# Performance work log

Measured on AMD Instinct MI355X. Metric: run time of the kernel, lower is better.

The kernel has to match this reference:

```python
import jax, jax.numpy as jnp
import numpy as np
from jax import lax

EPS = 1e-5
NPOINT, NSAMPLE = 1024, 32

def bn(x, g, b, m, v):
    # inference-mode batchnorm over last (channel) axis
    return (x - m) * (g * lax.rsqrt(v + EPS)) + b

def gather_pts(points, idx):
    # points [B,N,C], idx [B,...] -> [B,...,C]
    return jax.vmap(lambda p, i: p[i])(points, idx)

def fps(xyz, npoint):
    # iterative farthest point sampling, deterministic start at index 0
    B, N, _ = xyz.shape
    xyz = lax.stop_gradient(xyz)
    def step(carry, _):
        dist, far = carry
        centroid = jnp.take_along_axis(xyz, far[:, None, None], axis=1)  # [B,1,3]
        d = jnp.sum((xyz - centroid) ** 2, -1)                           # [B,N]
        dist = jnp.minimum(dist, d)
        return (dist, jnp.argmax(dist, -1)), far
    init = (jnp.full((B, N), 1e10, xyz.dtype), jnp.zeros((B,), jnp.int32))
    _, idxs = lax.scan(step, init, None, length=npoint)
    return idxs.T  # [B,npoint]

def setup_inputs():
    key = jax.random.key(0)
    ks = jax.random.split(key, 8)
    d = {"x": jax.random.normal(ks[0], (8, 8192, 3), jnp.float32)}
    d["conv1_w"] = jax.random.normal(ks[1], (64, 3), jnp.float32) * 0.3
    d["conv2_w"] = jax.random.normal(ks[2], (64, 64), jnp.float32) * 0.1
    d["lconv1_w"] = jax.random.normal(ks[3], (128, 128), jnp.float32) * 0.08
    d["lconv2_w"] = jax.random.normal(ks[4], (128, 128), jnp.float32) * 0.08
    for name, c, k in (("bn1", 64, ks[5]), ("bn2", 64, ks[6]), ("lbn1", 128, ks[7]), ("lbn2", 128, jax.random.fold_in(key, 99))):
        d[name + "_g"] = jax.random.uniform(k, (c,), jnp.float32, 0.5, 1.5)
        d[name + "_b"] = jax.random.normal(jax.random.fold_in(k, 1), (c,), jnp.float32) * 0.1
        d[name + "_m"] = jnp.zeros((c,), jnp.float32)
        d[name + "_v"] = jnp.ones((c,), jnp.float32)
    return d

def reference(x, conv1_w, conv2_w, lconv1_w, lconv2_w,
              bn1_g, bn1_b, bn1_m, bn1_v, bn2_g, bn2_b, bn2_m, bn2_v,
              lbn1_g, lbn1_b, lbn1_m, lbn1_v, lbn2_g, lbn2_b, lbn2_m, lbn2_v):
    xyz = x[..., :3]                                                    # [B,N,3]
    f = jax.nn.relu(bn(jnp.einsum("bnd,ed->bne", x, conv1_w), bn1_g, bn1_b, bn1_m, bn1_v))
    f = jax.nn.relu(bn(jnp.einsum("bne,fe->bnf", f, conv2_w), bn2_g, bn2_b, bn2_m, bn2_v))  # [B,N,64]
    # sample_and_group(npoint=1024, nsample=32)
    fps_idx = fps(xyz, NPOINT)                                          # [B,S]
    new_xyz = gather_pts(xyz, fps_idx)                                  # [B,S,3]
    new_pts = gather_pts(f, fps_idx)                                    # [B,S,64]
    d2 = (jnp.sum(new_xyz ** 2, -1)[:, :, None] + jnp.sum(xyz ** 2, -1)[:, None, :]
          - 2.0 * jnp.einsum("bsd,bnd->bsn", new_xyz, xyz))             # [B,S,N]
    knn_idx = lax.top_k(-d2, NSAMPLE)[1]                                # [B,S,K] smallest dists
    grouped = gather_pts(f, knn_idx)                                    # [B,S,K,64]
    centered = grouped - new_pts[:, :, None, :]
    feat = jnp.concatenate([centered, jnp.broadcast_to(new_pts[:, :, None, :], grouped.shape)], -1)  # [B,S,K,128]
    # Local_op: two 1x1 conv + BN + relu, max over K
    h = jax.nn.relu(bn(jnp.einsum("bskd,ed->bske", feat, lconv1_w), lbn1_g, lbn1_b, lbn1_m, lbn1_v))
    h = jax.nn.relu(bn(jnp.einsum("bske,fe->bskf", h, lconv2_w), lbn2_g, lbn2_b, lbn2_m, lbn2_v))
    feature_0 = jnp.transpose(jnp.max(h, axis=2), (0, 2, 1))            # [B,128,S]
    return (new_xyz, feature_0, new_xyz, feature_0)
```

## Files before the change

kernel.cpp:

```cpp
#include <hip/hip_runtime.h>
#include <hip/hip_bf16.h>
#include <math.h>
#include <stdint.h>

#define EPS_BN 1e-5f

constexpr int Nx = 8192;
constexpr int NP = 1024;
constexpr int NWORK = 248;
constexpr int NEMB  = 128;
#define POISON_I ((int)0xAAAAAAAA)

typedef __attribute__((ext_vector_type(8))) __bf16 bf16x8;
typedef __attribute__((ext_vector_type(4))) float  f32x4;
typedef __attribute__((ext_vector_type(2))) float  f32x2;
typedef unsigned int uint32;
typedef unsigned long long u64;

template<int CTRL, int RMASK>
__device__ __forceinline__ u64 dpp_max_u64(u64 k) {
    uint32 klo = (uint32)k, khi = (uint32)(k >> 32);
    uint32 plo = (uint32)__builtin_amdgcn_update_dpp((int)klo, (int)klo, CTRL, RMASK, 0xf, false);
    uint32 phi = (uint32)__builtin_amdgcn_update_dpp((int)khi, (int)khi, CTRL, RMASK, 0xf, false);
    u64 p = ((u64)phi << 32) | plo;
    return (p > k) ? p : k;
}
__device__ __forceinline__ u64 wave_max_u64(u64 k) {
    k = dpp_max_u64<0x111, 0xf>(k);
    k = dpp_max_u64<0x112, 0xf>(k);
    k = dpp_max_u64<0x114, 0xf>(k);
    k = dpp_max_u64<0x118, 0xf>(k);
    k = dpp_max_u64<0x142, 0xa>(k);
    k = dpp_max_u64<0x143, 0xc>(k);
    uint32 rlo = (uint32)__builtin_amdgcn_readlane((int)(uint32)k, 63);
    uint32 rhi = (uint32)__builtin_amdgcn_readlane((int)(k >> 32), 63);
    return ((u64)rhi << 32) | rlo;
}
template<int CTRL, int RMASK>
__device__ __forceinline__ int dpp_sum_i32(int c) {
    int t = __builtin_amdgcn_update_dpp(0, c, CTRL, RMASK, 0xf, true);
    return c + t;
}
__device__ __forceinline__ int wave_sum_i32(int c) {
    c = dpp_sum_i32<0x111, 0xf>(c);
    c = dpp_sum_i32<0x112, 0xf>(c);
    c = dpp_sum_i32<0x114, 0xf>(c);
    c = dpp_sum_i32<0x118, 0xf>(c);
    c = dpp_sum_i32<0x142, 0xa>(c);
    c = dpp_sum_i32<0x143, 0xc>(c);
    return __builtin_amdgcn_readlane(c, 63);
}
template<int CTRL, int RMASK>
__device__ __forceinline__ int dpp_min_i32(int v) {
    int t = __builtin_amdgcn_update_dpp(v, v, CTRL, RMASK, 0xf, false);
    return min(v, t);
}
__device__ __forceinline__ int wave_min_i32(int v) {
    v = dpp_min_i32<0x111, 0xf>(v);
    v = dpp_min_i32<0x112, 0xf>(v);
    v = dpp_min_i32<0x114, 0xf>(v);
    v = dpp_min_i32<0x118, 0xf>(v);
    v = dpp_min_i32<0x142, 0xa>(v);
    v = dpp_min_i32<0x143, 0xc>(v);
    return __builtin_amdgcn_readlane(v, 63);
}

__global__ __launch_bounds__(512, 1) void mega_kernel(
    const float* __restrict__ x,
    const float* __restrict__ w1, const float* __restrict__ w2,
    const float* g1, const float* b1, const float* m1, const float* v1,
    const float* g2, const float* b2, const float* m2, const float* v2,
    const float* __restrict__ lw1, const float* __restrict__ lw2,
    const float* lg1, const float* lb1, const float* lm1, const float* lv1,
    const float* lg2, const float* lb2, const float* lm2, const float* lv2,
    float* __restrict__ f, float4* __restrict__ pts4, int* fpsI, int* done,
    float* __restrict__ out0, float* __restrict__ out1,
    float* __restrict__ out2, float* __restrict__ out3)
{
    __shared__ __attribute__((aligned(16))) char smemRaw[131200];
    int tid = threadIdx.x;

    if (blockIdx.x < 8) {
#pragma clang fp contract(off)
        float4* xyzL = (float4*)smemRaw;
        u64*    redK = (u64*)(smemRaw + 131072);
        int b = blockIdx.x;
        int wid = tid >> 6, lane = tid & 63;
        const float* xb = x + (size_t)b * Nx * 3;
        f32x2 px[8], py[8], pz[8], dist[8];
        {
            const float4* xv = (const float4*)(xb + tid * 48);
            float F[48];
#pragma unroll
            for (int q = 0; q < 12; q++) {
                float4 v = xv[q];
                F[q*4+0]=v.x; F[q*4+1]=v.y; F[q*4+2]=v.z; F[q*4+3]=v.w;
            }
#pragma unroll
            for (int i = 0; i < 8; i++) {
                px[i] = (f32x2){F[(2*i)*3+0], F[(2*i+1)*3+0]};
                py[i] = (f32x2){F[(2*i)*3+1], F[(2*i+1)*3+1]};
                pz[i] = (f32x2){F[(2*i)*3+2], F[(2*i+1)*3+2]};
                dist[i] = (f32x2){1e10f, 1e10f};
            }
#pragma unroll
            for (int j = 0; j < 16; j++) {
                int jj = (j + (tid & 15)) & 15;
                xyzL[tid*16 + jj] = make_float4(F[jj*3], F[jj*3+1], F[jj*3+2], 0.f);
            }
        }
        __syncthreads();
        int far = 0;
        for (int st = 0; st < NP; st++) {
            float4 c = xyzL[far];
            if (tid == 0) {
                __hip_atomic_store(&fpsI[b*NP + st], far, __ATOMIC_RELAXED, __HIP_MEMORY_SCOPE_AGENT);
                int o = (b*NP + st) * 3;
                out0[o]=c.x; out0[o+1]=c.y; out0[o+2]=c.z;
                out2[o]=c.x; out2[o+1]=c.y; out2[o+2]=c.z;
            }
            f32x2 cx = {c.x, c.x}, cy = {c.y, c.y}, cz = {c.z, c.z};
            f32x2 bv2 = {-1.0f, -1.0f};
#pragma unroll
            for (int i = 0; i < 8; i++) {
                f32x2 dx = px[i] - cx, dy = py[i] - cy, dz = pz[i] - cz;
                f32x2 sq = (dx*dx + dy*dy) + dz*dz;
                f32x2 dm = __builtin_elementwise_min(dist[i], sq);
                dist[i] = dm;
                bv2 = __builtin_elementwise_max(bv2, dm);
            }
            float bv = fmaxf(bv2.x, bv2.y);
            int bi = 0;
#pragma unroll
            for (int i = 7; i >= 0; i--) {
                if (dist[i].y == bv) bi = tid*16 + 2*i + 1;
                if (dist[i].x == bv) bi = tid*16 + 2*i;
            }
            u64 bk = ((u64)__float_as_uint(bv) << 32) | (uint32)(~bi);
            bk = wave_max_u64(bk);
            if (lane == 0) redK[(st & 1)*8 + wid] = bk;
            __syncthreads();
            u64 mx = redK[(st & 1)*8 + 0];
#pragma unroll
            for (int i = 1; i < 8; i++) {
                u64 t2 = redK[(st & 1)*8 + i];
                if (t2 > mx) mx = t2;
            }
            far = (int)(~(uint32)mx);
        }
        return;
    }

    int wb = (int)blockIdx.x - 8;

    if (wb < NEMB) {
        float*  W1L = (float*)smemRaw;
        float4* W2L = (float4*)(smemRaw + 1024);
        float*  s1L = (float*)(smemRaw + 17408);
        float*  m1L = (float*)(smemRaw + 17664);
        float*  b1L = (float*)(smemRaw + 17920);
        float*  s2L = (float*)(smemRaw + 18176);
        float*  m2L = (float*)(smemRaw + 18432);
        float*  b2L = (float*)(smemRaw + 18688);
        if (tid < 192) W1L[tid] = w1[tid];
        for (int i = tid; i < 1024; i += 512) W2L[i] = ((const float4*)w2)[i];
        if (tid < 64) {
            s1L[tid] = g1[tid] * (1.0f / sqrtf(v1[tid] + EPS_BN));
            m1L[tid] = m1[tid];  b1L[tid] = b1[tid];
            s2L[tid] = g2[tid] * (1.0f / sqrtf(v2[tid] + EPS_BN));
            m2L[tid] = m2[tid];  b2L[tid] = b2[tid];
        }
        __syncthreads();
        int n = wb * 512 + tid;
        const float* xp = x + (size_t)n * 3;
        float x0 = xp[0], x1 = xp[1], x2 = xp[2];
        {
#pragma clang fp contract(off)
            float nv = (x0 * x0 + x1 * x1) + x2 * x2;
            pts4[n] = make_float4(x0, x1, x2, nv);
        }
        float t[64];
#pragma unroll
        for (int e = 0; e < 64; e++) {
            float v = fmaf(x2, W1L[e*3+2], fmaf(x1, W1L[e*3+1], x0 * W1L[e*3]));
            v = (v - m1L[e]) * s1L[e] + b1L[e];
            t[e] = fmaxf(v, 0.0f);
        }
        float acc[64];
#pragma unroll
        for (int o = 0; o < 64; o++) acc[o] = 0.0f;
#pragma unroll
        for (int e4 = 0; e4 < 16; e4++) {
            float a0 = t[e4*4], a1 = t[e4*4+1], a2 = t[e4*4+2], a3 = t[e4*4+3];
#pragma unroll
            for (int o = 0; o < 64; o++) {
                float4 w = W2L[o*16 + e4];
                acc[o] = fmaf(a3, w.w, fmaf(a2, w.z, fmaf(a1, w.y, fmaf(a0, w.x, acc[o]))));
            }
        }
        float4* fo = (float4*)(f + (size_t)n * 64);
#pragma unroll
        for (int q = 0; q < 16; q++) {
            float r0 = fmaxf((acc[q*4+0] - m2L[q*4+0]) * s2L[q*4+0] + b2L[q*4+0], 0.f);
            float r1 = fmaxf((acc[q*4+1] - m2L[q*4+1]) * s2L[q*4+1] + b2L[q*4+1], 0.f);
            float r2 = fmaxf((acc[q*4+2] - m2L[q*4+2]) * s2L[q*4+2] + b2L[q*4+2], 0.f);
            float r3 = fmaxf((acc[q*4+3] - m2L[q*4+3]) * s2L[q*4+3] + b2L[q*4+3], 0.f);
            fo[q] = make_float4(r0, r1, r2, r3);
        }
        __syncthreads();
        if (tid == 0)
            __hip_atomic_fetch_add(done, 1, __ATOMIC_RELEASE, __HIP_MEMORY_SCOPE_AGENT);
    }

    __bf16* featL = (__bf16*)smemRaw;
    __bf16* h1L   = (__bf16*)(smemRaw + 8704);
    float*  cf    = (float*) (smemRaw + 17408);
    int*    rowL  = (int*)   (smemRaw + 17664);
    int*    redC  = (int*)   (smemRaw + 17792);
    int*    redM  = (int*)   (smemRaw + 17856);
    int*    misc  = (int*)   (smemRaw + 17920);

    int wv = tid >> 6, lane = tid & 63;
    int l15 = lane & 15, quad = lane >> 4;
    int nbase = wv * 16;
    const f32x4 vzero = {0.f, 0.f, 0.f, 0.f};

    bf16x8 bf1[4], bf2[4];
#pragma unroll
    for (int kt = 0; kt < 4; kt++) {
        const float* p1 = lw1 + (size_t)(nbase + l15) * 128 + kt*32 + quad*8;
        const float* p2 = lw2 + (size_t)(nbase + l15) * 128 + kt*32 + quad*8;
        bf16x8 a1, a2;
#pragma unroll
        for (int j = 0; j < 8; j++) { a1[j] = (__bf16)p1[j]; a2[j] = (__bf16)p2[j]; }
        bf1[kt] = a1; bf2[kt] = a2;
    }
    int oc = nbase + l15;
    float sc1 = lg1[oc] * (1.0f / sqrtf(lv1[oc] + EPS_BN));
    float mm1 = lm1[oc], bb1 = lb1[oc];
    float sc2 = lg2[oc] * (1.0f / sqrtf(lv2[oc] + EPS_BN));
    float mm2 = lm2[oc], bb2 = lb2[oc];

    if (tid == 0) {
        while (__hip_atomic_load(done, __ATOMIC_RELAXED, __HIP_MEMORY_SCOPE_AGENT) != POISON_I + NEMB)
            __builtin_amdgcn_s_sleep(8);
    }
    __syncthreads();
    __threadfence();

    for (int t = wb; t < 8192; t += NWORK) {
        int b = t & 7, s = t >> 3;
        int q = (b << 10) | s;
        if (tid == 0) {
            int v;
            while ((v = __hip_atomic_load(&fpsI[q], __ATOMIC_RELAXED, __HIP_MEMORY_SCOPE_AGENT)) < 0)
                __builtin_amdgcn_s_sleep(2);
            misc[1] = v;
            misc[0] = 0;
        }
        __syncthreads();
        int cIdx = misc[1];
        if (tid < 16) {
            float4 v = *(const float4*)(f + ((size_t)b * Nx + cIdx) * 64 + tid * 4);
            cf[tid*4]=v.x; cf[tid*4+1]=v.y; cf[tid*4+2]=v.z; cf[tid*4+3]=v.w;
        }
        uint32 key[16];
        {
#pragma clang fp contract(off)
            const float4* P = pts4 + (size_t)b * Nx;
            float4 qp = P[cIdx];
#pragma unroll
            for (int i = 0; i < 16; i++) {
                int n = tid + (i << 9);
                float4 p = P[n];
                float dot = (qp.x * p.x + qp.y * p.y) + qp.z * p.z;
                float d = (qp.w + p.w) - 2.0f * dot;
                uint32 u = __float_as_uint(d);
                key[i] = (u & 0x80000000u) ? ~u : (u | 0x80000000u);
            }
        }
        uint32 prefix = 0; int krem = 32;
        for (int bit = 31; bit >= 0; bit--) {
            uint32 sv = prefix >> bit;
            int cnt = 0;
#pragma unroll
            for (int i = 0; i < 16; i++)
                cnt += ((key[i] >> bit) == sv) ? 1 : 0;
            cnt = wave_sum_i32(cnt);
            if (lane == 0) redC[(bit & 1)*8 + wv] = cnt;
            __syncthreads();
            int total = 0;
#pragma unroll
            for (int j = 0; j < 8; j++) total += redC[(bit & 1)*8 + j];
            if (total < krem) { prefix |= (1u << bit); krem -= total; }
        }
#pragma unroll
        for (int i = 0; i < 16; i++) {
            if (key[i] < prefix) {
                int pos = atomicAdd(&misc[0], 1);
                rowL[pos] = tid + (i << 9);
            }
        }
        __syncthreads();
        int last = -1;
        for (int tt = 0; tt < krem; tt++) {
            int local = 0x7fffffff;
#pragma unroll
            for (int i = 0; i < 16; i++) {
                int n = tid + (i << 9);
                if (key[i] == prefix && n > last && n < local) local = n;
            }
            local = wave_min_i32(local);
            if (lane == 0) redM[(tt & 1)*8 + wv] = local;
            __syncthreads();
            int g = 0x7fffffff;
#pragma unroll
            for (int j = 0; j < 8; j++) g = min(g, redM[(tt & 1)*8 + j]);
            if (tid == 0) rowL[32 - krem + tt] = g;
            last = g;
        }
        __syncthreads();
        {
            int k = tid >> 4, j0 = (tid & 15) * 4;
            int nbr = rowL[k];
            float4 v = *(const float4*)(f + ((size_t)b * Nx + nbr) * 64 + j0);
            float c0 = cf[j0], c1 = cf[j0+1], c2 = cf[j0+2], c3 = cf[j0+3];
            __bf16* dl = featL + k * 136 + j0;
            dl[0]=(__bf16)(v.x-c0); dl[1]=(__bf16)(v.y-c1); dl[2]=(__bf16)(v.z-c2); dl[3]=(__bf16)(v.w-c3);
            __bf16* dr = dl + 64;
            dr[0]=(__bf16)c0; dr[1]=(__bf16)c1; dr[2]=(__bf16)c2; dr[3]=(__bf16)c3;
        }
        __syncthreads();
        f32x4 acc[2];
        acc[0] = vzero; acc[1] = vzero;
#pragma unroll
        for (int mt = 0; mt < 2; mt++)
#pragma unroll
            for (int kt = 0; kt < 4; kt++) {
                bf16x8 a = *(const bf16x8*)(featL + (mt*16 + l15) * 136 + kt*32 + quad*8);
                acc[mt] = __builtin_amdgcn_mfma_f32_16x16x32_bf16(a, bf1[kt], acc[mt], 0, 0, 0);
            }
#pragma unroll
        for (int mt = 0; mt < 2; mt++)
#pragma unroll
            for (int rj = 0; rj < 4; rj++) {
                float h = fmaxf((acc[mt][rj] - mm1) * sc1 + bb1, 0.0f);
                h1L[(mt*16 + quad*4 + rj) * 136 + oc] = (__bf16)h;
            }
        __syncthreads();
        acc[0] = vzero; acc[1] = vzero;
#pragma unroll
        for (int mt = 0; mt < 2; mt++)
#pragma unroll
            for (int kt = 0; kt < 4; kt++) {
                bf16x8 a = *(const bf16x8*)(h1L + (mt*16 + l15) * 136 + kt*32 + quad*8);
                acc[mt] = __builtin_amdgcn_mfma_f32_16x16x32_bf16(a, bf2[kt], acc[mt], 0, 0, 0);
            }
        float vmx = 0.0f;
#pragma unroll
        for (int mt = 0; mt < 2; mt++)
#pragma unroll
            for (int rj = 0; rj < 4; rj++) {
                float h = fmaxf((acc[mt][rj] - mm2) * sc2 + bb2, 0.0f);
                vmx = fmaxf(vmx, h);
            }
        vmx = fmaxf(vmx, __shfl_xor(vmx, 16));
        vmx = fmaxf(vmx, __shfl_xor(vmx, 32));
        if (quad == 0) {
            size_t off = (size_t)b * (128*1024) + (size_t)oc * 1024 + s;
            out1[off] = vmx;
            out3[off] = vmx;
        }
        __syncthreads();
    }
}

extern "C" void kernel_launch(void* const* d_in, const int* in_sizes, int n_in,
                              void* d_out, int out_size, void* d_ws, size_t ws_size,
                              hipStream_t stream)
{
    const float* x    = (const float*)d_in[0];
    const float* c1w  = (const float*)d_in[1];
    const float* c2w  = (const float*)d_in[2];
    const float* l1w  = (const float*)d_in[3];
    const float* l2w  = (const float*)d_in[4];
    const float* bn1g = (const float*)d_in[5];
    const float* bn1b = (const float*)d_in[6];
    const float* bn1m = (const float*)d_in[7];
    const float* bn1v = (const float*)d_in[8];
    const float* bn2g = (const float*)d_in[9];
    const float* bn2b = (const float*)d_in[10];
    const float* bn2m = (const float*)d_in[11];
    const float* bn2v = (const float*)d_in[12];
    const float* lb1g = (const float*)d_in[13];
    const float* lb1b = (const float*)d_in[14];
    const float* lb1m = (const float*)d_in[15];
    const float* lb1v = (const float*)d_in[16];
    const float* lb2g = (const float*)d_in[17];
    const float* lb2b = (const float*)d_in[18];
    const float* lb2m = (const float*)d_in[19];
    const float* lb2v = (const float*)d_in[20];

    float* out = (float*)d_out;
    char* ws = (char*)d_ws;
    float*  f    = (float*)(ws);
    float4* pts4 = (float4*)(ws + 16777216);
    int*    fpsI = (int*)   (ws + 17825792);
    int*    done = (int*)   (ws + 17858560);

    float* out0 = out;
    float* out1 = out + 24576;
    float* out2 = out + 1073152;
    float* out3 = out + 1097728;

    mega_kernel<<<256, 512, 0, stream>>>(x, c1w, c2w,
        bn1g, bn1b, bn1m, bn1v, bn2g, bn2b, bn2m, bn2v,
        l1w, l2w, lb1g, lb1b, lb1m, lb1v, lb2g, lb2b, lb2m, lb2v,
        f, pts4, fpsI, done, out0, out1, out2, out3);
}
```

Baseline: 1.102 ms.

## Bucket FPS points spatially and skip distance updates for far-away thread clusters

The FPS blocks now counting-sort the 8192 points into a 512-cell Morton-ordered grid, so each thread owns 16 spatially close points. Each thread stores its cluster centroid and radius and skips the per-point min-distance update when a triangle-inequality bound shows the new centroid cannot lower any of its distances. The cross-wave max reduction is also replaced with a DPP reduction over the eight wave results. The cost is extra setup (atomics, scan, index indirection through posOf), a per-step sqrt and branch, and more registers. The skip relies on conservative fudge factors to keep the chosen indices and tie-breaking exact.

```diff
diff --git a/kernel.cpp b/kernel.cpp
--- a/kernel.cpp
+++ b/kernel.cpp
@@ -15,6 +15,7 @@
 typedef __attribute__((ext_vector_type(4))) float  f32x4;
 typedef __attribute__((ext_vector_type(2))) float  f32x2;
 typedef unsigned int uint32;
+typedef unsigned short u16;
 typedef unsigned long long u64;
 
 template<int CTRL, int RMASK>
@@ -49,6 +50,15 @@
     c = dpp_sum_i32<0x142, 0xa>(c);
     c = dpp_sum_i32<0x143, 0xc>(c);
     return __builtin_amdgcn_readlane(c, 63);
+}
+__device__ __forceinline__ int wave_scan_incl_i32(int v) {
+    v += __builtin_amdgcn_update_dpp(0, v, 0x111, 0xf, 0xf, true);
+    v += __builtin_amdgcn_update_dpp(0, v, 0x112, 0xf, 0xf, true);
+    v += __builtin_amdgcn_update_dpp(0, v, 0x114, 0xf, 0xf, true);
+    v += __builtin_amdgcn_update_dpp(0, v, 0x118, 0xf, 0xf, true);
+    v += __builtin_amdgcn_update_dpp(0, v, 0x142, 0xa, 0xf, true);
+    v += __builtin_amdgcn_update_dpp(0, v, 0x143, 0xc, 0xf, true);
+    return v;
 }
 template<int CTRL, int RMASK>
 __device__ __forceinline__ int dpp_min_i32(int v) {
@@ -77,76 +87,129 @@
     float* __restrict__ out0, float* __restrict__ out1,
     float* __restrict__ out2, float* __restrict__ out3)
 {
-    __shared__ __attribute__((aligned(16))) char smemRaw[131200];
+    __shared__ __attribute__((aligned(16))) char smemRaw[149664];
     int tid = threadIdx.x;
 
     if (blockIdx.x < 8) {
 #pragma clang fp contract(off)
-        float4* xyzL = (float4*)smemRaw;
-        u64*    redK = (u64*)(smemRaw + 131072);
+        float4* xyzL  = (float4*)smemRaw;
+        u16*    posOf = (u16*)  (smemRaw + 131072);
+        int*    cnts  = (int*)  (smemRaw + 147456);
+        int*    wsum  = (int*)  (smemRaw + 149504);
+        u64*    redK  = (u64*)  (smemRaw + 149536);
         int b = blockIdx.x;
         int wid = tid >> 6, lane = tid & 63;
         const float* xb = x + (size_t)b * Nx * 3;
-        f32x2 px[8], py[8], pz[8], dist[8];
+        float F[48];
         {
             const float4* xv = (const float4*)(xb + tid * 48);
-            float F[48];
 #pragma unroll
             for (int q = 0; q < 12; q++) {
                 float4 v = xv[q];
                 F[q*4+0]=v.x; F[q*4+1]=v.y; F[q*4+2]=v.z; F[q*4+3]=v.w;
             }
-#pragma unroll
-            for (int i = 0; i < 8; i++) {
-                px[i] = (f32x2){F[(2*i)*3+0], F[(2*i+1)*3+0]};
-                py[i] = (f32x2){F[(2*i)*3+1], F[(2*i+1)*3+1]};
-                pz[i] = (f32x2){F[(2*i)*3+2], F[(2*i+1)*3+2]};
-                dist[i] = (f32x2){1e10f, 1e10f};
-            }
-#pragma unroll
-            for (int j = 0; j < 16; j++) {
-                int jj = (j + (tid & 15)) & 15;
-                xyzL[tid*16 + jj] = make_float4(F[jj*3], F[jj*3+1], F[jj*3+2], 0.f);
-            }
-        }
-        __syncthreads();
+        }
+        int bkt[16];
+#pragma unroll
+        for (int j = 0; j < 16; j++) {
+            int bx = (int)fminf(fmaxf(F[j*3+0] + 4.0f, 0.0f), 7.0f);
+            int by = (int)fminf(fmaxf(F[j*3+1] + 4.0f, 0.0f), 7.0f);
+            int bz = (int)fminf(fmaxf(F[j*3+2] + 4.0f, 0.0f), 7.0f);
+            bkt[j] = (bx&1) | ((by&1)<<1) | ((bz&1)<<2)
+                   | ((bx&2)<<2) | ((by&2)<<3) | ((bz&2)<<4)
+                   | ((bx&4)<<4) | ((by&4)<<5) | ((bz&4)<<6);
+        }
+        if (tid < 512) cnts[tid] = 0;
+        __syncthreads();
+#pragma unroll
+        for (int j = 0; j < 16; j++) atomicAdd(&cnts[bkt[j]], 1);
+        __syncthreads();
+        {
+            int v = cnts[tid];
+            int incl = wave_scan_incl_i32(v);
+            int tot = __builtin_amdgcn_readlane(incl, 63);
+            if (lane == 0) wsum[wid] = tot;
+            __syncthreads();
+            int off = 0;
+            for (int j = 0; j < 8; j++) off += (j < wid) ? wsum[j] : 0;
+            cnts[tid] = incl - v + off;
+        }
+        __syncthreads();
+#pragma unroll
+        for (int j = 0; j < 16; j++) {
+            int pos = atomicAdd(&cnts[bkt[j]], 1);
+            xyzL[pos] = make_float4(F[j*3], F[j*3+1], F[j*3+2], __int_as_float(tid*16 + j));
+            posOf[tid*16 + j] = (u16)pos;
+        }
+        __syncthreads();
+        float qx[16], qy[16], qz[16];
+        int   qi[16];
+        float gx = 0.f, gy = 0.f, gz = 0.f;
+#pragma unroll
+        for (int j0 = 0; j0 < 16; j0++) {
+            int j = (j0 + (tid & 15)) & 15;
+            float4 v = xyzL[tid*16 + j];
+            qx[j]=v.x; qy[j]=v.y; qz[j]=v.z; qi[j]=__float_as_int(v.w);
+            gx += v.x; gy += v.y; gz += v.z;
+        }
+        gx *= 0.0625f; gy *= 0.0625f; gz *= 0.0625f;
+        f32x2 px[8], py[8], pz[8], dist[8];
+        float r2m = 0.f;
+#pragma unroll
+        for (int i = 0; i < 8; i++) {
+            px[i] = (f32x2){qx[2*i], qx[2*i+1]};
+            py[i] = (f32x2){qy[2*i], qy[2*i+1]};
+            pz[i] = (f32x2){qz[2*i], qz[2*i+1]};
+            dist[i] = (f32x2){1e10f, 1e10f};
+            f32x2 rx = px[i] - (f32x2){gx,gx}, ry = py[i] - (f32x2){gy,gy}, rz = pz[i] - (f32x2){gz,gz};
+            f32x2 r2 = (rx*rx + ry*ry) + rz*rz;
+            r2m = fmaxf(r2m, fmaxf(r2.x, r2.y));
+        }
+        float r_hi = sqrtf(r2m) * 1.0001f + 1e-6f;
+        float s_my = 1e9f;
+        u64 mykey = 0;
         int far = 0;
         for (int st = 0; st < NP; st++) {
-            float4 c = xyzL[far];
+            int pos = posOf[far];
+            float4 c = xyzL[pos];
             if (tid == 0) {
                 __hip_atomic_store(&fpsI[b*NP + st], far, __ATOMIC_RELAXED, __HIP_MEMORY_SCOPE_AGENT);
                 int o = (b*NP + st) * 3;
                 out0[o]=c.x; out0[o+1]=c.y; out0[o+2]=c.z;
                 out2[o]=c.x; out2[o+1]=c.y; out2[o+2]=c.z;
             }
-            f32x2 cx = {c.x, c.x}, cy = {c.y, c.y}, cz = {c.z, c.z};
-            f32x2 bv2 = {-1.0f, -1.0f};
-#pragma unroll
-            for (int i = 0; i < 8; i++) {
-                f32x2 dx = px[i] - cx, dy = py[i] - cy, dz = pz[i] - cz;
-                f32x2 sq = (dx*dx + dy*dy) + dz*dz;
-                f32x2 dm = __builtin_elementwise_min(dist[i], sq);
-                dist[i] = dm;
-                bv2 = __builtin_elementwise_max(bv2, dm);
-            }
-            float bv = fmaxf(bv2.x, bv2.y);
-            int bi = 0;
-#pragma unroll
-            for (int i = 7; i >= 0; i--) {
-                if (dist[i].y == bv) bi = tid*16 + 2*i + 1;
-                if (dist[i].x == bv) bi = tid*16 + 2*i;
-            }
-            u64 bk = ((u64)__float_as_uint(bv) << 32) | (uint32)(~bi);
-            bk = wave_max_u64(bk);
+            float dcx = c.x - gx, dcy = c.y - gy, dcz = c.z - gz;
+            float dc2 = dcx*dcx + dcy*dcy + dcz*dcz;
+            float act = sqrtf(dc2) * 0.9999f - r_hi;
+            if (!(act > s_my)) {
+                f32x2 cx = {c.x, c.x}, cy = {c.y, c.y}, cz = {c.z, c.z};
+                f32x2 mx2 = {-1.0f, -1.0f};
+#pragma unroll
+                for (int i = 0; i < 8; i++) {
+                    f32x2 dx = px[i] - cx, dy = py[i] - cy, dz = pz[i] - cz;
+                    f32x2 sq = (dx*dx + dy*dy) + dz*dz;
+                    f32x2 dm = __builtin_elementwise_min(dist[i], sq);
+                    dist[i] = dm;
+                    mx2 = __builtin_elementwise_max(mx2, dm);
+                }
+                float bv = fmaxf(mx2.x, mx2.y);
+                int bi = 0x7fffffff;
+#pragma unroll
+                for (int i = 0; i < 8; i++) {
+                    if (dist[i].x == bv) bi = min(bi, qi[2*i]);
+                    if (dist[i].y == bv) bi = min(bi, qi[2*i+1]);
+                }
+                mykey = ((u64)__float_as_uint(bv) << 32) | (uint32)(~bi);
+                s_my = sqrtf(bv) * 1.0001f + 1e-6f;
+            }
+            u64 bk = wave_max_u64(mykey);
             if (lane == 0) redK[(st & 1)*8 + wid] = bk;
             __syncthreads();
-            u64 mx = redK[(st & 1)*8 + 0];
-#pragma unroll
-            for (int i = 1; i < 8; i++) {
-                u64 t2 = redK[(st & 1)*8 + i];
-                if (t2 > mx) mx = t2;
-            }
-            far = (int)(~(uint32)mx);
+            u64 k8 = redK[(st & 1)*8 + (lane & 7)];
+            k8 = dpp_max_u64<0x111, 0xf>(k8);
+            k8 = dpp_max_u64<0x112, 0xf>(k8);
+            k8 = dpp_max_u64<0x114, 0xf>(k8);
+            far = (int)(~(uint32)__builtin_amdgcn_readlane((int)(uint32)k8, 7));
         }
         return;
     }
```

Result: slower. 1.326 ms (+20.3%).
